# Performance work log

Hardware: AMD Instinct MI355X
Metric: run time of the kernel (lower is better)

## Reference

```python
import jax, jax.numpy as jnp
import numpy as np

R, N, IN_F, OUT_F = 8, 4096, 64, 64


def setup_inputs() -> dict:
    key = jax.random.key(0)
    k_adj, k_x, k_w = jax.random.split(key, 3)
    adjacency = jax.random.uniform(k_adj, (R, N, N), dtype=jnp.float32)
    x = jax.random.normal(k_x, (N, IN_F), dtype=jnp.float32)
    weight = jax.random.uniform(k_w, (R, OUT_F, IN_F), dtype=jnp.float32)
    return {"adjacency": adjacency, "x": x, "weight": weight}


def reference(adjacency, x, weight):
    # y = sum_r (A[r] @ x) @ W[r].T
    # messages: [R, N, IN_F]
    msgs = jnp.einsum("rnm,mi->rni", adjacency, x)
    # transform per relation and sum over relations: [N, OUT_F]
    y = jnp.einsum("rni,roi->no", msgs, weight)
    return y
```

## Files before the change

### kernel.cpp

```cpp
#include <hip/hip_runtime.h>
#include <hip/hip_bf16.h>

#define RR 8
#define NN 4096
#define FF 64

typedef float f32x4 __attribute__((ext_vector_type(4)));
typedef short bf16x8 __attribute__((ext_vector_type(8)));

__device__ __forceinline__ short f2b(float f) {
  __hip_bfloat16 h = __float2bfloat16(f);
  return __builtin_bit_cast(short, h);
}

__device__ __forceinline__ bf16x8 cvt8(f32x4 lo, f32x4 hi) {
  bf16x8 r;
  r[0] = f2b(lo[0]); r[1] = f2b(lo[1]); r[2] = f2b(lo[2]); r[3] = f2b(lo[3]);
  r[4] = f2b(hi[0]); r[5] = f2b(hi[1]); r[6] = f2b(hi[2]); r[7] = f2b(hi[3]);
  return r;
}

__global__ __launch_bounds__(256) void zero_out(float4* __restrict__ out) {
  out[blockIdx.x * 256 + threadIdx.x] = make_float4(0.f, 0.f, 0.f, 0.f);
}

__global__ __launch_bounds__(256) void compute_zt(const float* __restrict__ x,
                                                  const float* __restrict__ w,
                                                  short* __restrict__ zt) {
  const int tid   = threadIdx.x;
  const int lane  = tid & 63;
  const int wv    = tid >> 6;
  const int row16 = lane & 15;
  const int quad  = lane >> 4;
  const int r     = blockIdx.y;
  const int m0    = blockIdx.x * 64 + wv * 16;

  bf16x8 bfr[2];
#pragma unroll
  for (int s = 0; s < 2; ++s) {
    const float* p = x + (size_t)(m0 + row16) * FF + s * 32 + quad * 8;
    bfr[s] = cvt8(*(const f32x4*)p, *(const f32x4*)(p + 4));
  }

  f32x4 acc[4] = {{0.f,0.f,0.f,0.f},{0.f,0.f,0.f,0.f},
                  {0.f,0.f,0.f,0.f},{0.f,0.f,0.f,0.f}};
#pragma unroll
  for (int og = 0; og < 4; ++og) {
#pragma unroll
    for (int s = 0; s < 2; ++s) {
      const float* p = w + ((size_t)r * FF + og * 16 + row16) * FF + s * 32 + quad * 8;
      bf16x8 afr = cvt8(*(const f32x4*)p, *(const f32x4*)(p + 4));
      acc[og] = __builtin_amdgcn_mfma_f32_16x16x32_bf16(afr, bfr[s], acc[og], 0, 0, 0);
    }
  }

#pragma unroll
  for (int og = 0; og < 4; ++og)
#pragma unroll
    for (int j = 0; j < 4; ++j) {
      int o = og * 16 + quad * 4 + j;
      int m = m0 + row16;
      zt[((size_t)r * FF + o) * NN + m] = f2b(acc[og][j]);
    }
}


struct Chunk {
  f32x4  alo[2], ahi[2];
  bf16x8 b[2][4];
};

__device__ __forceinline__ Chunk load_chunk(const float* __restrict__ aptr,
                                            const short* __restrict__ zbase,
                                            int row16, int k0) {
  Chunk c;
#pragma unroll
  for (int s = 0; s < 2; ++s) {
    const float* p = aptr + k0 + s * 32;
    c.alo[s] = *(const f32x4*)p;
    c.ahi[s] = *(const f32x4*)(p + 4);
#pragma unroll
    for (int cg = 0; cg < 4; ++cg) {
      c.b[s][cg] = *(const bf16x8*)(zbase + (size_t)(cg * 16 + row16) * NN + k0 + s * 32);
    }
  }
  return c;
}

__global__ __launch_bounds__(256) void rgcn_main(const float* __restrict__ adj,
                                                 const short* __restrict__ zt,
                                                 float* __restrict__ out) {
  const int tid   = threadIdx.x;
  const int lane  = tid & 63;
  const int wv    = tid >> 6;
  const int row16 = lane & 15;
  const int quad  = lane >> 4;

  const int nt    = blockIdx.x;
  const int rk    = blockIdx.y;
  const int r     = rk >> 1;
  const int half  = rk & 1;
  const int n0    = nt * 64;
  const int row   = n0 + wv * 16 + row16;

  const float* aptr  = adj + (size_t)r * NN * NN + (size_t)row * NN
                           + half * 2048 + quad * 8;
  const short* zbase = zt + (size_t)r * FF * NN + half * 2048 + quad * 8;

  f32x4 acc[4] = {{0.f,0.f,0.f,0.f},{0.f,0.f,0.f,0.f},
                  {0.f,0.f,0.f,0.f},{0.f,0.f,0.f,0.f}};

  Chunk cur = load_chunk(aptr, zbase, row16, 0);

  for (int k0 = 0; k0 < 2048; k0 += 64) {
    int kn = (k0 + 64 < 2048) ? (k0 + 64) : 0;
    Chunk nxt = load_chunk(aptr, zbase, row16, kn);

#pragma unroll
    for (int s = 0; s < 2; ++s) {
      bf16x8 afr = cvt8(cur.alo[s], cur.ahi[s]);
#pragma unroll
      for (int cg = 0; cg < 4; ++cg)
        acc[cg] = __builtin_amdgcn_mfma_f32_16x16x32_bf16(afr, cur.b[s][cg], acc[cg], 0, 0, 0);
    }
    cur = nxt;
  }

#pragma unroll
  for (int cg = 0; cg < 4; ++cg)
#pragma unroll
    for (int j = 0; j < 4; ++j) {
      int orow = n0 + wv * 16 + quad * 4 + j;
      int ocol = cg * 16 + row16;
      atomicAdd(out + (size_t)orow * FF + ocol, acc[cg][j]);
    }
}

extern "C" void kernel_launch(void* const* d_in, const int* in_sizes, int n_in,
                              void* d_out, int out_size, void* d_ws, size_t ws_size,
                              hipStream_t stream) {
  const float* adj = (const float*)d_in[0];
  const float* x   = (const float*)d_in[1];
  const float* w   = (const float*)d_in[2];
  float* out = (float*)d_out;
  short* zt  = (short*)d_ws;

  zero_out<<<dim3(NN * FF / (4 * 256)), 256, 0, stream>>>((float4*)out);
  compute_zt<<<dim3(NN / 64, RR), 256, 0, stream>>>(x, w, zt);
  rgcn_main<<<dim3(NN / 64, RR * 2), 256, 0, stream>>>(adj, zt, out);
}
```

Baseline: 749.4 us.

## Stage adjacency tiles through LDS with coalesced loads and replace atomics with partial reduction

The main kernel now loads 64x128 adjacency tiles with coalesced row-contiguous float4 loads, converts them to bf16, and stores them into double-buffered padded LDS. The next tile is prefetched in registers during the MFMA work, and B fragments are loaded in an interleaved pattern. Output atomics are replaced by per-split partial buffers in workspace plus a separate reduction kernel, which also removes the zeroing kernel. This adds LDS traffic, block-wide syncs and an extra launch, and it depends on the workspace being large enough at a 16MB offset.

```diff
diff --git a/kernel.cpp b/kernel.cpp
--- a/kernel.cpp
+++ b/kernel.cpp
@@ -18,10 +18,6 @@
   r[0] = f2b(lo[0]); r[1] = f2b(lo[1]); r[2] = f2b(lo[2]); r[3] = f2b(lo[3]);
   r[4] = f2b(hi[0]); r[5] = f2b(hi[1]); r[6] = f2b(hi[2]); r[7] = f2b(hi[3]);
   return r;
-}
-
-__global__ __launch_bounds__(256) void zero_out(float4* __restrict__ out) {
-  out[blockIdx.x * 256 + threadIdx.x] = make_float4(0.f, 0.f, 0.f, 0.f);
 }
 
 __global__ __launch_bounds__(256) void compute_zt(const float* __restrict__ x,
@@ -65,75 +61,116 @@
 }
 
 
-struct Chunk {
-  f32x4  alo[2], ahi[2];
-  bf16x8 b[2][4];
-};
+#define BK    128
+#define NSTG  16
+#define LROW  136
 
-__device__ __forceinline__ Chunk load_chunk(const float* __restrict__ aptr,
-                                            const short* __restrict__ zbase,
-                                            int row16, int k0) {
-  Chunk c;
+__device__ __forceinline__ void issueA(const float* __restrict__ abase,
+                                       int trow, int tcol, int s, f32x4* av) {
 #pragma unroll
-  for (int s = 0; s < 2; ++s) {
-    const float* p = aptr + k0 + s * 32;
-    c.alo[s] = *(const f32x4*)p;
-    c.ahi[s] = *(const f32x4*)(p + 4);
-#pragma unroll
-    for (int cg = 0; cg < 4; ++cg) {
-      c.b[s][cg] = *(const bf16x8*)(zbase + (size_t)(cg * 16 + row16) * NN + k0 + s * 32);
-    }
-  }
-  return c;
+  for (int i = 0; i < 8; ++i)
+    av[i] = *(const f32x4*)(abase + (size_t)(i * 8 + trow) * NN + s * BK + tcol);
 }
 
-__global__ __launch_bounds__(256) void rgcn_main(const float* __restrict__ adj,
-                                                 const short* __restrict__ zt,
-                                                 float* __restrict__ out) {
+__device__ __forceinline__ void writeA(short* __restrict__ buf,
+                                       int trow, int tcol, const f32x4* av) {
+#pragma unroll
+  for (int i = 0; i < 8; ++i) {
+    short4 wv4;
+    wv4.x = f2b(av[i][0]); wv4.y = f2b(av[i][1]);
+    wv4.z = f2b(av[i][2]); wv4.w = f2b(av[i][3]);
+    *(short4*)(buf + (i * 8 + trow) * LROW + tcol) = wv4;
+  }
+}
+
+__device__ __forceinline__ void loadB4(const short* __restrict__ zb, int k, bf16x8* b) {
+#pragma unroll
+  for (int cg = 0; cg < 4; ++cg)
+    b[cg] = *(const bf16x8*)(zb + (size_t)cg * 16 * NN + k);
+}
+
+__device__ __forceinline__ void mfma4(bf16x8 a, const bf16x8* b, f32x4* acc) {
+  acc[0] = __builtin_amdgcn_mfma_f32_16x16x32_bf16(a, b[0], acc[0], 0, 0, 0);
+  acc[1] = __builtin_amdgcn_mfma_f32_16x16x32_bf16(a, b[1], acc[1], 0, 0, 0);
+  acc[2] = __builtin_amdgcn_mfma_f32_16x16x32_bf16(a, b[2], acc[2], 0, 0, 0);
+  acc[3] = __builtin_amdgcn_mfma_f32_16x16x32_bf16(a, b[3], acc[3], 0, 0, 0);
+}
+
+__global__ __launch_bounds__(256, 3) void rgcn_main(const float* __restrict__ adj,
+                                                    const short* __restrict__ zt,
+                                                    float* __restrict__ partial) {
+  __shared__ short lds[2][64 * LROW];
+
   const int tid   = threadIdx.x;
   const int lane  = tid & 63;
   const int wv    = tid >> 6;
   const int row16 = lane & 15;
   const int quad  = lane >> 4;
 
-  const int nt    = blockIdx.x;
-  const int rk    = blockIdx.y;
-  const int r     = rk >> 1;
-  const int half  = rk & 1;
-  const int n0    = nt * 64;
-  const int row   = n0 + wv * 16 + row16;
+  const int nt   = blockIdx.x;
+  const int rk   = blockIdx.y;
+  const int r    = rk >> 1;
+  const int half = rk & 1;
+  const int n0   = nt * 64;
 
-  const float* aptr  = adj + (size_t)r * NN * NN + (size_t)row * NN
-                           + half * 2048 + quad * 8;
-  const short* zbase = zt + (size_t)r * FF * NN + half * 2048 + quad * 8;
+  const int trow = tid >> 5;
+  const int tcol = (tid & 31) * 4;
+
+  const float* abase = adj + (size_t)r * NN * NN + (size_t)n0 * NN + half * 2048;
+  const short* zb    = zt + (size_t)r * FF * NN + (size_t)row16 * NN
+                          + half * 2048 + quad * 8;
 
   f32x4 acc[4] = {{0.f,0.f,0.f,0.f},{0.f,0.f,0.f,0.f},
                   {0.f,0.f,0.f,0.f},{0.f,0.f,0.f,0.f}};
+  f32x4 av[8];
 
-  Chunk cur = load_chunk(aptr, zbase, row16, 0);
+  issueA(abase, trow, tcol, 0, av);
+  writeA(&lds[0][0], trow, tcol, av);
+  issueA(abase, trow, tcol, 1, av);
+  __syncthreads();
 
-  for (int k0 = 0; k0 < 2048; k0 += 64) {
-    int kn = (k0 + 64 < 2048) ? (k0 + 64) : 0;
-    Chunk nxt = load_chunk(aptr, zbase, row16, kn);
+#pragma unroll 1
+  for (int s = 0; s < NSTG; ++s) {
+    const short* fb = &lds[s & 1][(wv * 16 + row16) * LROW + quad * 8];
 
-#pragma unroll
-    for (int s = 0; s < 2; ++s) {
-      bf16x8 afr = cvt8(cur.alo[s], cur.ahi[s]);
-#pragma unroll
-      for (int cg = 0; cg < 4; ++cg)
-        acc[cg] = __builtin_amdgcn_mfma_f32_16x16x32_bf16(afr, cur.b[s][cg], acc[cg], 0, 0, 0);
+    bf16x8 b0[4], b1[4];
+    loadB4(zb, s * BK,      b0);
+    loadB4(zb, s * BK + 32, b1);
+
+    bf16x8 a0 = *(const bf16x8*)(fb + 0);
+    mfma4(a0, b0, acc);
+    loadB4(zb, s * BK + 64, b0);
+    bf16x8 a1 = *(const bf16x8*)(fb + 32);
+    mfma4(a1, b1, acc);
+    loadB4(zb, s * BK + 96, b1);
+    bf16x8 a2 = *(const bf16x8*)(fb + 64);
+    mfma4(a2, b0, acc);
+    bf16x8 a3 = *(const bf16x8*)(fb + 96);
+    mfma4(a3, b1, acc);
+
+    if (s < NSTG - 1) {
+      writeA(&lds[(s + 1) & 1][0], trow, tcol, av);
+      if (s < NSTG - 2) issueA(abase, trow, tcol, s + 2, av);
+      __syncthreads();
     }
-    cur = nxt;
   }
 
+  float* pb = partial + ((size_t)rk * NN + n0) * FF;
 #pragma unroll
   for (int cg = 0; cg < 4; ++cg)
 #pragma unroll
-    for (int j = 0; j < 4; ++j) {
-      int orow = n0 + wv * 16 + quad * 4 + j;
-      int ocol = cg * 16 + row16;
-      atomicAdd(out + (size_t)orow * FF + ocol, acc[cg][j]);
-    }
+    for (int j = 0; j < 4; ++j)
+      pb[(size_t)(wv * 16 + quad * 4 + j) * FF + cg * 16 + row16] = acc[cg][j];
+}
+
+__global__ __launch_bounds__(256) void reduce_partials(const f32x4* __restrict__ p,
+                                                       f32x4* __restrict__ out) {
+  const int idx = blockIdx.x * 256 + threadIdx.x;
+  f32x4 s = {0.f, 0.f, 0.f, 0.f};
+#pragma unroll
+  for (int rk = 0; rk < 16; ++rk)
+    s += p[(size_t)rk * (NN * FF / 4) + idx];
+  out[idx] = s;
 }
 
 extern "C" void kernel_launch(void* const* d_in, const int* in_sizes, int n_in,
@@ -143,9 +180,12 @@
   const float* x   = (const float*)d_in[1];
   const float* w   = (const float*)d_in[2];
   float* out = (float*)d_out;
-  short* zt  = (short*)d_ws;
 
-  zero_out<<<dim3(NN * FF / (4 * 256)), 256, 0, stream>>>((float4*)out);
+  short* zt      = (short*)d_ws;
+  float* partial = (float*)((char*)d_ws + (16u << 20));
+
   compute_zt<<<dim3(NN / 64, RR), 256, 0, stream>>>(x, w, zt);
-  rgcn_main<<<dim3(NN / 64, RR * 2), 256, 0, stream>>>(adj, zt, out);
+  rgcn_main<<<dim3(NN / 64, RR * 2), 256, 0, stream>>>(adj, zt, partial);
+  reduce_partials<<<dim3(NN * FF / 4 / 256), 256, 0, stream>>>(
+      (const f32x4*)partial, (f32x4*)out);
 }
```

Result: faster. 729.1 us (-2.7%).
